# Kernel optimization log

Hardware: AMD Instinct MI355X
Metric: run time of the kernel (lower is better)

Reference implementation:

```python
import jax, jax.numpy as jnp
import numpy as np
import math

Z, H, G, S = 4, 16, 4, 4096          # batch, q heads, kv groups, seq len
BLOCK = 32                            # compression block size
NB = S // BLOCK                       # number of compressed KV blocks (128)
DQK, DV = 128, 128                    # head dims


def setup_inputs() -> dict:
    key = jax.random.key(0)
    k1, k2, k3 = jax.random.split(key, 3)
    q = jax.random.normal(k1, (Z, H, S, DQK), jnp.float32)
    k_blocks = jax.random.normal(k2, (Z, G, NB, DQK), jnp.float32)
    v_blocks = jax.random.normal(k3, (Z, G, NB, DV), jnp.float32)
    # block j covers tokens [j*BLOCK, (j+1)*BLOCK), so it 'ends' at position (j+1)*BLOCK-1
    block_ends = (jnp.arange(1, NB + 1) * BLOCK - 1).astype(jnp.int32)
    return {"q": q, "k_blocks": k_blocks, "v_blocks": v_blocks, "block_ends": block_ends}


def reference(q, k_blocks, v_blocks, block_ends):
    """NSA compression attention fwd: block-end causal masking over compressed KV blocks.
    q: [Z,H,S,Dqk]; k_blocks/v_blocks: [Z,G,NB,D]; block_ends: [NB] int.
    Query at position m attends to compressed block j iff block_ends[j] <= m.
    Rows with no valid block output zeros (matching the kernel's l_i==0 path)."""
    Zb, Hb, Sb, Dq = q.shape
    Gb = k_blocks.shape[1]
    sm_scale = 1.0 / math.sqrt(Dq)
    # GQA: head h -> kv group h // (H // G)
    qg = (q * sm_scale).reshape(Zb, Gb, Hb // Gb, Sb, Dq)
    s = jnp.einsum('zghsd,zgnd->zghsn', qg, k_blocks)        # [Z,G,H/G,S,NB]
    pos = jnp.arange(Sb)
    mask = block_ends[None, :] <= pos[:, None]               # [S,NB]
    s_masked = jnp.where(mask, s, -jnp.inf)
    m = jnp.max(s_masked, axis=-1, keepdims=True)            # online-softmax max (M)
    m_safe = jnp.where(jnp.isfinite(m), m, 0.0)
    p = jnp.where(mask, jnp.exp(s_masked - jax.lax.stop_gradient(m_safe)), 0.0)
    l = jnp.sum(p, axis=-1, keepdims=True)                   # softmax denom (exp(L-M))
    o = jnp.einsum('zghsn,zgnv->zghsv', p, v_blocks)
    o = jnp.where(l > 0, o / jnp.where(l > 0, l, 1.0), 0.0)
    return o.reshape(Zb, Hb, Sb, -1)                         # [Z,H,S,Dv]
```

## Files before the change

kernel.cpp:

```cpp
#include <hip/hip_runtime.h>
#include <hip/hip_bf16.h>


#define Zc 4
#define Hc 16
#define Gc 4
#define Sc 4096
#define NBc 128
#define Dc 128

typedef __attribute__((ext_vector_type(8))) short short8;
typedef __attribute__((ext_vector_type(4))) float float4v;

__device__ inline short f2bf(float f) {
    union { float f; unsigned u; } x; x.f = f;
    unsigned r = (x.u + 0x7fffu + ((x.u >> 16) & 1u)) >> 16;
    return (short)r;
}

__global__ __launch_bounds__(256, 2)
void nsa_fwd(const float* __restrict__ q, const float* __restrict__ kb,
             const float* __restrict__ vb, float* __restrict__ out) {
    __shared__ __align__(16) short Ksh[NBc * Dc];
    __shared__ __align__(16) short Vt[Dc * NBc];

    const int m0   = blockIdx.x * 128;
    const int h    = blockIdx.y;
    const int z    = blockIdx.z;
    const int g    = h >> 2;
    const int tid  = threadIdx.x;
    const int wave = tid >> 6;
    const int lane = tid & 63;
    const int l16  = lane & 15;
    const int quad = lane >> 4;

    const float* ksrc = kb + ((size_t)(z * Gc + g)) * NBc * Dc;
    for (int i = tid; i < NBc * Dc / 8; i += 256) {
        const float4v* p = (const float4v*)(ksrc + (size_t)i * 8);
        float4v f0 = p[0], f1 = p[1];
        short8 o;
        o[0]=f2bf(f0[0]); o[1]=f2bf(f0[1]); o[2]=f2bf(f0[2]); o[3]=f2bf(f0[3]);
        o[4]=f2bf(f1[0]); o[5]=f2bf(f1[1]); o[6]=f2bf(f1[2]); o[7]=f2bf(f1[3]);
        ((short8*)Ksh)[i] = o;
    }
    const float* vsrc = vb + ((size_t)(z * Gc + g)) * NBc * Dc;
    for (int i = tid; i < NBc * Dc / 4; i += 256) {
        int c = i >> 7;
        int n = i & 127;
        float4v f = *(const float4v*)(vsrc + (size_t)n * Dc + c * 4);
        Vt[(c * 4 + 0) * NBc + n] = f2bf(f[0]);
        Vt[(c * 4 + 1) * NBc + n] = f2bf(f[1]);
        Vt[(c * 4 + 2) * NBc + n] = f2bf(f[2]);
        Vt[(c * 4 + 3) * NBc + n] = f2bf(f[3]);
    }
    __syncthreads();

    const float sm_scale = 0.08838834764831845f;
    const int row_base = wave * 32;
    const float* qtile = q + (((size_t)(z * Hc + h)) * Sc + m0) * Dc;

    float4v acc[2][8];
    #pragma unroll
    for (int t = 0; t < 2; t++)
        #pragma unroll
        for (int c = 0; c < 8; c++) acc[t][c] = (float4v)0.f;

    #pragma unroll
    for (int kbi = 0; kbi < 4; kbi++) {
        const int d0 = kbi * 32 + quad * 8;
        short8 afrag[2];
        #pragma unroll
        for (int t = 0; t < 2; t++) {
            const float* src = qtile + (size_t)(row_base + t * 16 + l16) * Dc + d0;
            float4v f0 = *(const float4v*)src;
            float4v f1 = *(const float4v*)(src + 4);
            short8 a;
            a[0]=f2bf(f0[0]*sm_scale); a[1]=f2bf(f0[1]*sm_scale);
            a[2]=f2bf(f0[2]*sm_scale); a[3]=f2bf(f0[3]*sm_scale);
            a[4]=f2bf(f1[0]*sm_scale); a[5]=f2bf(f1[1]*sm_scale);
            a[6]=f2bf(f1[2]*sm_scale); a[7]=f2bf(f1[3]*sm_scale);
            afrag[t] = a;
        }
        #pragma unroll
        for (int c = 0; c < 8; c++) {
            short8 bfrag = *(const short8*)(Ksh + (c * 16 + l16) * Dc + d0);
            #pragma unroll
            for (int t = 0; t < 2; t++)
                acc[t][c] = __builtin_amdgcn_mfma_f32_16x16x32_bf16(
                    afrag[t], bfrag, acc[t][c], 0, 0, 0);
        }
    }

    float inv_l[2][4];
    #pragma unroll
    for (int t = 0; t < 2; t++) {
        #pragma unroll
        for (int r = 0; r < 4; r++) {
            const int mg = m0 + row_base + t * 16 + quad * 4 + r;
            int nvalid = (mg + 1) >> 5;
            if (nvalid > NBc) nvalid = NBc;
            float mx = -1e30f;
            #pragma unroll
            for (int c = 0; c < 8; c++) {
                const int j = c * 16 + l16;
                float s = (j < nvalid) ? acc[t][c][r] : -1e30f;
                acc[t][c][r] = s;
                mx = fmaxf(mx, s);
            }
            #pragma unroll
            for (int off = 1; off < 16; off <<= 1)
                mx = fmaxf(mx, __shfl_xor(mx, off, 64));
            float lsum = 0.f;
            #pragma unroll
            for (int c = 0; c < 8; c++) {
                float s = acc[t][c][r];
                float p = (s > -1e29f) ? __expf(s - mx) : 0.f;
                acc[t][c][r] = p;
                lsum += p;
            }
            #pragma unroll
            for (int off = 1; off < 16; off <<= 1)
                lsum += __shfl_xor(lsum, off, 64);
            inv_l[t][r] = (lsum > 0.f) ? 1.f / lsum : 0.f;
        }
    }

    __syncthreads();
    short* P = Ksh;
    #pragma unroll
    for (int t = 0; t < 2; t++)
        #pragma unroll
        for (int c = 0; c < 8; c++)
            #pragma unroll
            for (int r = 0; r < 4; r++)
                P[(row_base + t * 16 + quad * 4 + r) * NBc + c * 16 + l16] =
                    f2bf(acc[t][c][r]);
    __syncthreads();

    float4v oacc[2][8];
    #pragma unroll
    for (int t = 0; t < 2; t++)
        #pragma unroll
        for (int c = 0; c < 8; c++) oacc[t][c] = (float4v)0.f;

    #pragma unroll
    for (int kbi = 0; kbi < 4; kbi++) {
        const int b0 = kbi * 32 + quad * 8;
        short8 afrag[2];
        #pragma unroll
        for (int t = 0; t < 2; t++)
            afrag[t] = *(const short8*)(P + (row_base + t * 16 + l16) * NBc + b0);
        #pragma unroll
        for (int c = 0; c < 8; c++) {
            short8 bfrag = *(const short8*)(Vt + (c * 16 + l16) * NBc + b0);
            #pragma unroll
            for (int t = 0; t < 2; t++)
                oacc[t][c] = __builtin_amdgcn_mfma_f32_16x16x32_bf16(
                    afrag[t], bfrag, oacc[t][c], 0, 0, 0);
        }
    }

    float* otile = out + (((size_t)(z * Hc + h)) * Sc + m0) * Dc;
    #pragma unroll
    for (int t = 0; t < 2; t++)
        #pragma unroll
        for (int r = 0; r < 4; r++) {
            const int row = row_base + t * 16 + quad * 4 + r;
            const float s = inv_l[t][r];
            #pragma unroll
            for (int c = 0; c < 8; c++)
                otile[(size_t)row * Dc + c * 16 + l16] = oacc[t][c][r] * s;
        }
}

extern "C" void kernel_launch(void* const* d_in, const int* in_sizes, int n_in,
                              void* d_out, int out_size, void* d_ws, size_t ws_size,
                              hipStream_t stream) {
    const float* q  = (const float*)d_in[0];
    const float* kb = (const float*)d_in[1];
    const float* vb = (const float*)d_in[2];
    float* out = (float*)d_out;
    dim3 grid(Sc / 128, Hc, Zc);
    nsa_fwd<<<grid, dim3(256), 0, stream>>>(q, kb, vb, out);
}
```

Before: 290.4 us.

## Keep P in registers via transposed S MFMA and drop K shared staging

Computes S transposed (K as the A operand, Q as B) so each lane holds one query row's scores, and reduces softmax with two cross-quad shuffles. The probabilities are packed to bf16 and redistributed with lane shuffles as the A fragment for PV, which removes the P round trip through LDS and one barrier. K is read straight from global memory instead of being staged in LDS, V^T is padded to limit bank conflicts, and LDS use drops enough to allow 4 blocks per CU. Normalisation is applied to P before PV, and bf16 conversion becomes round-half-up with perm packing, which changes rounding slightly.

```diff
diff --git a/kernel.cpp b/kernel.cpp
--- a/kernel.cpp
+++ b/kernel.cpp
@@ -1,5 +1,4 @@
 #include <hip/hip_runtime.h>
-#include <hip/hip_bf16.h>
 
 
 #define Zc 4
@@ -8,168 +7,173 @@
 #define Sc 4096
 #define NBc 128
 #define Dc 128
+#define VST 136
 
 typedef __attribute__((ext_vector_type(8))) short short8;
 typedef __attribute__((ext_vector_type(4))) float float4v;
 
-__device__ inline short f2bf(float f) {
-    union { float f; unsigned u; } x; x.f = f;
-    unsigned r = (x.u + 0x7fffu + ((x.u >> 16) & 1u)) >> 16;
-    return (short)r;
+__device__ inline unsigned pk2bf(float a, float b) {
+    union { float f; unsigned u; } x, y; x.f = a; y.f = b;
+    return __builtin_amdgcn_perm(y.u + 0x8000u, x.u + 0x8000u, 0x07060302u);
 }
 
-__global__ __launch_bounds__(256, 2)
+__device__ inline short8 mkfrag(float4v f0, float4v f1) {
+    union { short8 v; unsigned d[4]; } u;
+    u.d[0] = pk2bf(f0[0], f0[1]);
+    u.d[1] = pk2bf(f0[2], f0[3]);
+    u.d[2] = pk2bf(f1[0], f1[1]);
+    u.d[3] = pk2bf(f1[2], f1[3]);
+    return u.v;
+}
+
+__global__ __launch_bounds__(256, 4)
 void nsa_fwd(const float* __restrict__ q, const float* __restrict__ kb,
              const float* __restrict__ vb, float* __restrict__ out) {
-    __shared__ __align__(16) short Ksh[NBc * Dc];
-    __shared__ __align__(16) short Vt[Dc * NBc];
+    __shared__ __align__(16) short Vt[Dc * VST];
 
     const int m0   = blockIdx.x * 128;
     const int h    = blockIdx.y;
     const int z    = blockIdx.z;
     const int g    = h >> 2;
     const int tid  = threadIdx.x;
-    const int wave = tid >> 6;
+    const int wq   = tid >> 6;
     const int lane = tid & 63;
     const int l16  = lane & 15;
     const int quad = lane >> 4;
 
-    const float* ksrc = kb + ((size_t)(z * Gc + g)) * NBc * Dc;
-    for (int i = tid; i < NBc * Dc / 8; i += 256) {
-        const float4v* p = (const float4v*)(ksrc + (size_t)i * 8);
-        float4v f0 = p[0], f1 = p[1];
-        short8 o;
-        o[0]=f2bf(f0[0]); o[1]=f2bf(f0[1]); o[2]=f2bf(f0[2]); o[3]=f2bf(f0[3]);
-        o[4]=f2bf(f1[0]); o[5]=f2bf(f1[1]); o[6]=f2bf(f1[2]); o[7]=f2bf(f1[3]);
-        ((short8*)Ksh)[i] = o;
+    const float* vsrc = vb + (size_t)(z * Gc + g) * NBc * Dc;
+    #pragma unroll
+    for (int it = 0; it < 16; it++) {
+        int i = it * 256 + tid;
+        int c = i >> 7, n = i & 127;
+        float4v f = *(const float4v*)(vsrc + (size_t)n * Dc + c * 4);
+        #pragma unroll
+        for (int k2 = 0; k2 < 4; k2++) {
+            union { float f; unsigned u; } x; x.f = f[k2];
+            Vt[(c * 4 + k2) * VST + n] = (short)((x.u + 0x8000u) >> 16);
+        }
     }
-    const float* vsrc = vb + ((size_t)(z * Gc + g)) * NBc * Dc;
-    for (int i = tid; i < NBc * Dc / 4; i += 256) {
-        int c = i >> 7;
-        int n = i & 127;
-        float4v f = *(const float4v*)(vsrc + (size_t)n * Dc + c * 4);
-        Vt[(c * 4 + 0) * NBc + n] = f2bf(f[0]);
-        Vt[(c * 4 + 1) * NBc + n] = f2bf(f[1]);
-        Vt[(c * 4 + 2) * NBc + n] = f2bf(f[2]);
-        Vt[(c * 4 + 3) * NBc + n] = f2bf(f[3]);
-    }
-    __syncthreads();
 
-    const float sm_scale = 0.08838834764831845f;
-    const int row_base = wave * 32;
-    const float* qtile = q + (((size_t)(z * Hc + h)) * Sc + m0) * Dc;
+    const float* ksrc  = kb + (size_t)(z * Gc + g) * NBc * Dc;
+    const float* qbase = q + ((size_t)(z * Hc + h) * Sc + m0 + wq * 32) * Dc;
 
-    float4v acc[2][8];
+    float4v acc[8][2];
     #pragma unroll
-    for (int t = 0; t < 2; t++)
+    for (int c = 0; c < 8; c++)
         #pragma unroll
-        for (int c = 0; c < 8; c++) acc[t][c] = (float4v)0.f;
+        for (int t = 0; t < 2; t++) acc[c][t] = (float4v)0.f;
 
     #pragma unroll
-    for (int kbi = 0; kbi < 4; kbi++) {
-        const int d0 = kbi * 32 + quad * 8;
-        short8 afrag[2];
+    for (int dk = 0; dk < 4; dk++) {
+        const int d0 = dk * 32 + quad * 8;
+        short8 bq[2];
         #pragma unroll
         for (int t = 0; t < 2; t++) {
-            const float* src = qtile + (size_t)(row_base + t * 16 + l16) * Dc + d0;
-            float4v f0 = *(const float4v*)src;
-            float4v f1 = *(const float4v*)(src + 4);
-            short8 a;
-            a[0]=f2bf(f0[0]*sm_scale); a[1]=f2bf(f0[1]*sm_scale);
-            a[2]=f2bf(f0[2]*sm_scale); a[3]=f2bf(f0[3]*sm_scale);
-            a[4]=f2bf(f1[0]*sm_scale); a[5]=f2bf(f1[1]*sm_scale);
-            a[6]=f2bf(f1[2]*sm_scale); a[7]=f2bf(f1[3]*sm_scale);
-            afrag[t] = a;
+            const float* s = qbase + (size_t)(t * 16 + l16) * Dc + d0;
+            bq[t] = mkfrag(*(const float4v*)s, *(const float4v*)(s + 4));
         }
         #pragma unroll
         for (int c = 0; c < 8; c++) {
-            short8 bfrag = *(const short8*)(Ksh + (c * 16 + l16) * Dc + d0);
+            const float* s = ksrc + (size_t)(c * 16 + l16) * Dc + d0;
+            short8 a = mkfrag(*(const float4v*)s, *(const float4v*)(s + 4));
             #pragma unroll
             for (int t = 0; t < 2; t++)
-                acc[t][c] = __builtin_amdgcn_mfma_f32_16x16x32_bf16(
-                    afrag[t], bfrag, acc[t][c], 0, 0, 0);
+                acc[c][t] = __builtin_amdgcn_mfma_f32_16x16x32_bf16(
+                    a, bq[t], acc[c][t], 0, 0, 0);
         }
     }
 
-    float inv_l[2][4];
+    const float sm_scale = 0.08838834764831845f;
+    unsigned Ppk[8][2][2];
     #pragma unroll
     for (int t = 0; t < 2; t++) {
+        const int mg = m0 + wq * 32 + t * 16 + l16;
+        int nv = (mg + 1) >> 5; if (nv > NBc) nv = NBc;
+        float mx = -1e30f;
         #pragma unroll
-        for (int r = 0; r < 4; r++) {
-            const int mg = m0 + row_base + t * 16 + quad * 4 + r;
-            int nvalid = (mg + 1) >> 5;
-            if (nvalid > NBc) nvalid = NBc;
-            float mx = -1e30f;
+        for (int c = 0; c < 8; c++)
             #pragma unroll
-            for (int c = 0; c < 8; c++) {
-                const int j = c * 16 + l16;
-                float s = (j < nvalid) ? acc[t][c][r] : -1e30f;
-                acc[t][c][r] = s;
+            for (int r = 0; r < 4; r++) {
+                const int j = c * 16 + quad * 4 + r;
+                float s = acc[c][t][r] * sm_scale;
+                s = (j < nv) ? s : -1e30f;
+                acc[c][t][r] = s;
                 mx = fmaxf(mx, s);
             }
+        mx = fmaxf(mx, __shfl_xor(mx, 16, 64));
+        mx = fmaxf(mx, __shfl_xor(mx, 32, 64));
+        float ls = 0.f;
+        #pragma unroll
+        for (int c = 0; c < 8; c++)
             #pragma unroll
-            for (int off = 1; off < 16; off <<= 1)
-                mx = fmaxf(mx, __shfl_xor(mx, off, 64));
-            float lsum = 0.f;
-            #pragma unroll
-            for (int c = 0; c < 8; c++) {
-                float s = acc[t][c][r];
+            for (int r = 0; r < 4; r++) {
+                float s = acc[c][t][r];
                 float p = (s > -1e29f) ? __expf(s - mx) : 0.f;
-                acc[t][c][r] = p;
-                lsum += p;
+                acc[c][t][r] = p;
+                ls += p;
             }
-            #pragma unroll
-            for (int off = 1; off < 16; off <<= 1)
-                lsum += __shfl_xor(lsum, off, 64);
-            inv_l[t][r] = (lsum > 0.f) ? 1.f / lsum : 0.f;
+        ls += __shfl_xor(ls, 16, 64);
+        ls += __shfl_xor(ls, 32, 64);
+        const float inv = (ls > 0.f) ? 1.f / ls : 0.f;
+        #pragma unroll
+        for (int c = 0; c < 8; c++) {
+            Ppk[c][t][0] = pk2bf(acc[c][t][0] * inv, acc[c][t][1] * inv);
+            Ppk[c][t][1] = pk2bf(acc[c][t][2] * inv, acc[c][t][3] * inv);
         }
     }
 
     __syncthreads();
-    short* P = Ksh;
+
+    float4v oacc[8][2];
+    #pragma unroll
+    for (int c = 0; c < 8; c++)
+        #pragma unroll
+        for (int t = 0; t < 2; t++) oacc[c][t] = (float4v)0.f;
+
+    const int s0 = (((2 * quad) & 3) << 4) | l16;
+    const int s1 = (((2 * quad + 1) & 3) << 4) | l16;
+    const bool hi = (quad >= 2);
+
+    #pragma unroll
+    for (int kbi = 0; kbi < 4; kbi++) {
+        short8 ap[2];
+        #pragma unroll
+        for (int t = 0; t < 2; t++) {
+            const int c1 = 2 * kbi;
+            unsigned w0a = (unsigned)__shfl((int)Ppk[c1    ][t][0], s0, 64);
+            unsigned w0b = (unsigned)__shfl((int)Ppk[c1 + 1][t][0], s0, 64);
+            unsigned w1a = (unsigned)__shfl((int)Ppk[c1    ][t][1], s0, 64);
+            unsigned w1b = (unsigned)__shfl((int)Ppk[c1 + 1][t][1], s0, 64);
+            unsigned w2a = (unsigned)__shfl((int)Ppk[c1    ][t][0], s1, 64);
+            unsigned w2b = (unsigned)__shfl((int)Ppk[c1 + 1][t][0], s1, 64);
+            unsigned w3a = (unsigned)__shfl((int)Ppk[c1    ][t][1], s1, 64);
+            unsigned w3b = (unsigned)__shfl((int)Ppk[c1 + 1][t][1], s1, 64);
+            union { short8 v; unsigned d[4]; } u;
+            u.d[0] = hi ? w0b : w0a;
+            u.d[1] = hi ? w1b : w1a;
+            u.d[2] = hi ? w2b : w2a;
+            u.d[3] = hi ? w3b : w3a;
+            ap[t] = u.v;
+        }
+        #pragma unroll
+        for (int c = 0; c < 8; c++) {
+            short8 bv = *(const short8*)(Vt + (c * 16 + l16) * VST + kbi * 32 + quad * 8);
+            #pragma unroll
+            for (int t = 0; t < 2; t++)
+                oacc[c][t] = __builtin_amdgcn_mfma_f32_16x16x32_bf16(
+                    ap[t], bv, oacc[c][t], 0, 0, 0);
+        }
+    }
+
+    float* obase = out + ((size_t)(z * Hc + h) * Sc + m0 + wq * 32) * Dc;
     #pragma unroll
     for (int t = 0; t < 2; t++)
         #pragma unroll
-        for (int c = 0; c < 8; c++)
-            #pragma unroll
-            for (int r = 0; r < 4; r++)
-                P[(row_base + t * 16 + quad * 4 + r) * NBc + c * 16 + l16] =
-                    f2bf(acc[t][c][r]);
-    __syncthreads();
-
-    float4v oacc[2][8];
-    #pragma unroll
-    for (int t = 0; t < 2; t++)
-        #pragma unroll
-        for (int c = 0; c < 8; c++) oacc[t][c] = (float4v)0.f;
-
-    #pragma unroll
-    for (int kbi = 0; kbi < 4; kbi++) {
-        const int b0 = kbi * 32 + quad * 8;
-        short8 afrag[2];
-        #pragma unroll
-        for (int t = 0; t < 2; t++)
-            afrag[t] = *(const short8*)(P + (row_base + t * 16 + l16) * NBc + b0);
-        #pragma unroll
-        for (int c = 0; c < 8; c++) {
-            short8 bfrag = *(const short8*)(Vt + (c * 16 + l16) * NBc + b0);
-            #pragma unroll
-            for (int t = 0; t < 2; t++)
-                oacc[t][c] = __builtin_amdgcn_mfma_f32_16x16x32_bf16(
-                    afrag[t], bfrag, oacc[t][c], 0, 0, 0);
-        }
-    }
-
-    float* otile = out + (((size_t)(z * Hc + h)) * Sc + m0) * Dc;
-    #pragma unroll
-    for (int t = 0; t < 2; t++)
-        #pragma unroll
-        for (int r = 0; r < 4; r++) {
-            const int row = row_base + t * 16 + quad * 4 + r;
-            const float s = inv_l[t][r];
+        for (int rr = 0; rr < 4; rr++) {
+            const int row = t * 16 + quad * 4 + rr;
             #pragma unroll
             for (int c = 0; c < 8; c++)
-                otile[(size_t)row * Dc + c * 16 + l16] = oacc[t][c][r] * s;
+                obase[(size_t)row * Dc + c * 16 + l16] = oacc[c][t][rr];
         }
 }
 
```

Result: no change. 296.1 us (+2.0%).
